# Optimization experiments

Measured on AMD Instinct MI355X. Metric: run time of the kernel, lower is better.

## Reference

```python
import jax, jax.numpy as jnp
import numpy as np

INPUT_LEN = 256
LATENT = 128
B, T = 64, 1024
# layer (in_dim, units): encoder: (256,256),(256,128); decoder: (128,256),(256,256)
LAYERS = [(INPUT_LEN, 2 * LATENT), (2 * LATENT, LATENT), (LATENT, 2 * LATENT), (2 * LATENT, INPUT_LEN)]


def _lstm_relu(xs, W, U, b):
    """Keras LSTM with activation='relu', recurrent_activation='sigmoid'.
    xs: [B,T,F]; W: [F,4H]; U: [H,4H]; b: [4H]; gate order i,f,g,o. Returns [B,T,H]."""
    Bsz = xs.shape[0]
    H = U.shape[0]
    h0 = jnp.zeros((Bsz, H), xs.dtype)
    c0 = jnp.zeros((Bsz, H), xs.dtype)
    # precompute input projection for all timesteps: [T,B,4H]
    zx = jnp.einsum('btf,fg->tbg', xs, W) + b

    def step(carry, zx_t):
        h, c = carry
        z = zx_t + h @ U
        i, f, g, o = jnp.split(z, 4, axis=-1)
        i = jax.nn.sigmoid(i)
        f = jax.nn.sigmoid(f)
        o = jax.nn.sigmoid(o)
        g = jax.nn.relu(g)
        c = f * c + i * g
        h = o * jax.nn.relu(c)
        return (h, c), h

    _, hs = jax.lax.scan(step, (h0, c0), zx)  # hs: [T,B,H]
    return jnp.swapaxes(hs, 0, 1)


def setup_inputs() -> dict:
    key = jax.random.key(0)
    ks = jax.random.split(key, 1 + 3 * len(LAYERS))
    d = {"x": jax.random.normal(ks[0], (B, T, INPUT_LEN), dtype=jnp.float32)}
    for li, (fin, h) in enumerate(LAYERS):
        kW, kU, kb = ks[1 + 3 * li], ks[2 + 3 * li], ks[3 + 3 * li]
        d[f"W{li+1}"] = jax.random.normal(kW, (fin, 4 * h), dtype=jnp.float32) * 0.05
        d[f"U{li+1}"] = jax.random.normal(kU, (h, 4 * h), dtype=jnp.float32) * 0.05
        d[f"b{li+1}"] = jnp.zeros((4 * h,), dtype=jnp.float32)
    return d


def reference(x, W1, U1, b1, W2, U2, b2, W3, U3, b3, W4, U4, b4):
    h = _lstm_relu(x, W1, U1, b1)   # encoder layer 1: [B,T,256]
    h = _lstm_relu(h, W2, U2, b2)   # encoder layer 2: [B,T,128]
    h = _lstm_relu(h, W3, U3, b3)   # decoder layer 1: [B,T,256]
    h = _lstm_relu(h, W4, U4, b4)   # decoder layer 2: [B,T,256]
    return h
```

## Files before the change

### kernel.cpp

```cpp
#include <hip/hip_runtime.h>
#include <hip/hip_bf16.h>


typedef __bf16 bf16x8 __attribute__((ext_vector_type(8)));
typedef float f32x4 __attribute__((ext_vector_type(4)));
typedef unsigned long long u64;

#define NWG 56
#define TSTEPS 1024
#define NSTEPS (TSTEPS + 3)

__device__ __forceinline__ f32x4 mfma16(bf16x8 a, bf16x8 b, f32x4 c) {
  return __builtin_amdgcn_mfma_f32_16x16x32_bf16(a, b, c, 0, 0, 0);
}

__device__ __forceinline__ float sigmoid_fast(float x) {
  return 1.0f / (1.0f + __expf(-x));
}

__device__ __forceinline__ bf16x8 load_frag_llc(const __bf16* p) {
  union { bf16x8 v; u64 d[2]; } u;
  u.d[0] = __hip_atomic_load((const u64*)p, __ATOMIC_RELAXED,
                             __HIP_MEMORY_SCOPE_AGENT);
  u.d[1] = __hip_atomic_load((const u64*)(p + 4), __ATOMIC_RELAXED,
                             __HIP_MEMORY_SCOPE_AGENT);
  return u.v;
}

__device__ __forceinline__ void store8_llc(__bf16* p, u64 v) {
  __hip_atomic_store((u64*)p, v, __ATOMIC_RELAXED, __HIP_MEMORY_SCOPE_AGENT);
}

__device__ __forceinline__ void poll_flags(unsigned* flags, unsigned s) {
  const int lane = threadIdx.x & 63;
  const int idx = (lane < NWG) ? lane : 0;
  while (true) {
    unsigned v = __hip_atomic_load(&flags[idx * 32], __ATOMIC_RELAXED,
                                   __HIP_MEMORY_SCOPE_AGENT);
    if (!__ballot(v < s)) break;
    __builtin_amdgcn_s_sleep(1);
  }
}

template <int F, int H, int LAYER>
__device__ void layer_loop(const float* __restrict__ xg,
                           const __bf16* __restrict__ xin,
                           const float* __restrict__ W,
                           const float* __restrict__ U,
                           const float* __restrict__ bias_g,
                           __bf16* __restrict__ hbuf,
                           float* __restrict__ out,
                           unsigned* flags, int wg, int slice, __bf16* smem) {
  constexpr int KW = F / 32;
  constexpr int KU = H / 32;
  constexpr int FOURH = 4 * H;
  const int tid = threadIdx.x;
  const int wave = tid >> 6;
  const int lane = tid & 63;
  const int l15 = lane & 15;
  const int q = lane >> 4;
  const int hcol = slice * 16 + l15;
  const int brow = wave * 16;

  float bz[4];
#pragma unroll
  for (int nt = 0; nt < 4; ++nt) bz[nt] = bias_g[nt * H + hcol];

  bf16x8 wf[4][KW];
  bf16x8 uf[4][KU];
  for (int idx = tid; idx < F * 64; idx += 256) {
    int k = idx >> 6, c = idx & 63;
    int col = (c >> 4) * H + slice * 16 + (c & 15);
    smem[c * F + k] = (__bf16)W[k * FOURH + col];
  }
  __syncthreads();
#pragma unroll
  for (int nt = 0; nt < 4; ++nt)
#pragma unroll
    for (int kk = 0; kk < KW; ++kk)
      wf[nt][kk] = *(const bf16x8*)&smem[(nt * 16 + l15) * F + kk * 32 + q * 8];
  __syncthreads();
  for (int idx = tid; idx < H * 64; idx += 256) {
    int k = idx >> 6, c = idx & 63;
    int col = (c >> 4) * H + slice * 16 + (c & 15);
    smem[c * H + k] = (__bf16)U[k * FOURH + col];
  }
  __syncthreads();
#pragma unroll
  for (int nt = 0; nt < 4; ++nt)
#pragma unroll
    for (int kk = 0; kk < KU; ++kk)
      uf[nt][kk] = *(const bf16x8*)&smem[(nt * 16 + l15) * H + kk * 32 + q * 8];
  __syncthreads();

  __bf16* hlds = smem;

  float c_state[4] = {0.f, 0.f, 0.f, 0.f};

  for (int s = 0; s < NSTEPS; ++s) {
    const int t = s - (LAYER - 1);
    const bool active = (t >= 0) & (t < TSTEPS);
    poll_flags(flags, (unsigned)s);
    float hv[4];
    if (active) {
      f32x4 acc[4] = {};
      if (LAYER == 1) {
        const float* xrow = xg + ((size_t)(brow + l15) * 1024 + t) * 256 + q * 8;
#pragma unroll
        for (int kk = 0; kk < KW; ++kk) {
          const float4* p = (const float4*)(xrow + kk * 32);
          float4 a0 = p[0], a1 = p[1];
          bf16x8 a;
          a[0] = (__bf16)a0.x; a[1] = (__bf16)a0.y;
          a[2] = (__bf16)a0.z; a[3] = (__bf16)a0.w;
          a[4] = (__bf16)a1.x; a[5] = (__bf16)a1.y;
          a[6] = (__bf16)a1.z; a[7] = (__bf16)a1.w;
#pragma unroll
          for (int nt = 0; nt < 4; ++nt) acc[nt] = mfma16(a, wf[nt][kk], acc[nt]);
        }
      } else {
        const __bf16* xr = xin + ((size_t)(t & 1) * 64 + brow + l15) * F + q * 8;
#pragma unroll
        for (int kk = 0; kk < KW; ++kk) {
          bf16x8 a = load_frag_llc(xr + kk * 32);
#pragma unroll
          for (int nt = 0; nt < 4; ++nt) acc[nt] = mfma16(a, wf[nt][kk], acc[nt]);
        }
      }
      if (t > 0) {
        const __bf16* hr = hbuf + ((size_t)((t - 1) & 1) * 64 + brow + l15) * H + q * 8;
#pragma unroll
        for (int kk = 0; kk < KU; ++kk) {
          bf16x8 a = load_frag_llc(hr + kk * 32);
#pragma unroll
          for (int nt = 0; nt < 4; ++nt) acc[nt] = mfma16(a, uf[nt][kk], acc[nt]);
        }
      }
#pragma unroll
      for (int r = 0; r < 4; ++r) {
        float zi = acc[0][r] + bz[0];
        float zf = acc[1][r] + bz[1];
        float zg = acc[2][r] + bz[2];
        float zo = acc[3][r] + bz[3];
        float ig = sigmoid_fast(zi);
        float fg = sigmoid_fast(zf);
        float gg = fmaxf(zg, 0.0f);
        float og = sigmoid_fast(zo);
        float cn = fg * c_state[r] + ig * gg;
        c_state[r] = cn;
        hv[r] = og * fmaxf(cn, 0.0f);
        hlds[(brow + q * 4 + r) * 16 + l15] = (__bf16)hv[r];
      }
    }
    __syncthreads();
    if (active) {
      int row = tid >> 2, cg = tid & 3;
      u64 v = *(const u64*)&hlds[row * 16 + cg * 4];
      store8_llc(hbuf + ((size_t)(t & 1) * 64 + row) * H + slice * 16 + cg * 4, v);
      if (LAYER == 4) {
#pragma unroll
        for (int r = 0; r < 4; ++r) {
          int b = brow + q * 4 + r;
          out[((size_t)b * 1024 + t) * 256 + hcol] = hv[r];
        }
      }
    }
    __syncthreads();
    if (tid == 0)
      __hip_atomic_store(&flags[wg * 32], (unsigned)(s + 1), __ATOMIC_RELAXED,
                         __HIP_MEMORY_SCOPE_AGENT);
  }
}

struct KParams {
  const float* x;
  const float* W1; const float* U1; const float* b1;
  const float* W2; const float* U2; const float* b2;
  const float* W3; const float* U3; const float* b3;
  const float* W4; const float* U4; const float* b4;
  float* out;
  unsigned* flags;
  void* h1; void* h2; void* h3; void* h4;
};

__global__ __launch_bounds__(256, 1) void lstm_kernel(KParams p) {
  __shared__ __align__(16) __bf16 smem[64 * 256];
  int wg = blockIdx.x;
  if (wg < 16)
    layer_loop<256, 256, 1>(p.x, nullptr, p.W1, p.U1, p.b1, (__bf16*)p.h1,
                            nullptr, p.flags, wg, wg, smem);
  else if (wg < 24)
    layer_loop<256, 128, 2>(nullptr, (const __bf16*)p.h1, p.W2, p.U2, p.b2,
                            (__bf16*)p.h2, nullptr, p.flags, wg, wg - 16, smem);
  else if (wg < 40)
    layer_loop<128, 256, 3>(nullptr, (const __bf16*)p.h2, p.W3, p.U3, p.b3,
                            (__bf16*)p.h3, nullptr, p.flags, wg, wg - 24, smem);
  else
    layer_loop<256, 256, 4>(nullptr, (const __bf16*)p.h3, p.W4, p.U4, p.b4,
                            (__bf16*)p.h4, p.out, p.flags, wg, wg - 40, smem);
}

extern "C" void kernel_launch(void* const* d_in, const int* in_sizes, int n_in,
                              void* d_out, int out_size, void* d_ws, size_t ws_size,
                              hipStream_t stream) {
  unsigned char* ws = (unsigned char*)d_ws;
  KParams p;
  p.x  = (const float*)d_in[0];
  p.W1 = (const float*)d_in[1];  p.U1 = (const float*)d_in[2];  p.b1 = (const float*)d_in[3];
  p.W2 = (const float*)d_in[4];  p.U2 = (const float*)d_in[5];  p.b2 = (const float*)d_in[6];
  p.W3 = (const float*)d_in[7];  p.U3 = (const float*)d_in[8];  p.b3 = (const float*)d_in[9];
  p.W4 = (const float*)d_in[10]; p.U4 = (const float*)d_in[11]; p.b4 = (const float*)d_in[12];
  p.out = (float*)d_out;
  p.flags = (unsigned*)ws;
  size_t off = 8192;
  p.h1 = (void*)(ws + off); off += (size_t)2 * 64 * 256 * 2;
  p.h2 = (void*)(ws + off); off += (size_t)2 * 64 * 128 * 2;
  p.h3 = (void*)(ws + off); off += (size_t)2 * 64 * 256 * 2;
  p.h4 = (void*)(ws + off);

  hipMemsetAsync(d_ws, 0, 8192, stream);

  lstm_kernel<<<dim3(NWG), dim3(256), 0, stream>>>(p);
}
```

Before: 8.022 ms.

## Narrow per-step barrier to neighbor layers, prefetch x, defer output stores

```diff
diff --git a/kernel.cpp b/kernel.cpp
--- a/kernel.cpp
+++ b/kernel.cpp
@@ -9,6 +9,9 @@
 #define NWG 56
 #define TSTEPS 1024
 #define NSTEPS (TSTEPS + 3)
+
+__device__ __constant__ const int kFlagCnt[6]  = {0, 16, 8, 16, 16, 0};
+__device__ __constant__ const int kFlagBase[6] = {0, 0, 32, 64, 96, 0};
 
 __device__ __forceinline__ f32x4 mfma16(bf16x8 a, bf16x8 b, f32x4 c) {
   return __builtin_amdgcn_mfma_f32_16x16x32_bf16(a, b, c, 0, 0, 0);
@@ -31,14 +34,25 @@
   __hip_atomic_store((u64*)p, v, __ATOMIC_RELAXED, __HIP_MEMORY_SCOPE_AGENT);
 }
 
-__device__ __forceinline__ void poll_flags(unsigned* flags, unsigned s) {
+template <int LAYER>
+__device__ __forceinline__ void wait_deps(unsigned* flags, unsigned s) {
+  constexpr int n1 = (LAYER >= 2) ? ((LAYER - 1 == 2) ? 8 : 16) : 0;
+  constexpr int n2 = (LAYER == 2) ? 8 : 16;
+  constexpr int n3 = (LAYER <= 3) ? ((LAYER + 1 == 2) ? 8 : 16) : 0;
+  constexpr int b1 = (LAYER >= 2) ? (LAYER - 2) * 32 : 0;
+  constexpr int b2 = (LAYER - 1) * 32;
+  constexpr int b3 = (LAYER <= 3) ? LAYER * 32 : 0;
   const int lane = threadIdx.x & 63;
-  const int idx = (lane < NWG) ? lane : 0;
+  int fidx;
+  if (lane < n1) fidx = b1 + lane;
+  else if (lane < n1 + n2) fidx = b2 + (lane - n1);
+  else if (lane < n1 + n2 + n3) fidx = b3 + (lane - n1 - n2);
+  else fidx = b2;
+  unsigned* p = &flags[fidx];
   while (true) {
-    unsigned v = __hip_atomic_load(&flags[idx * 32], __ATOMIC_RELAXED,
+    unsigned v = __hip_atomic_load(p, __ATOMIC_RELAXED,
                                    __HIP_MEMORY_SCOPE_AGENT);
     if (!__ballot(v < s)) break;
-    __builtin_amdgcn_s_sleep(1);
   }
 }
 
@@ -50,10 +64,11 @@
                            const float* __restrict__ bias_g,
                            __bf16* __restrict__ hbuf,
                            float* __restrict__ out,
-                           unsigned* flags, int wg, int slice, __bf16* smem) {
+                           unsigned* flags, int slice, __bf16* smem) {
   constexpr int KW = F / 32;
   constexpr int KU = H / 32;
   constexpr int FOURH = 4 * H;
+  constexpr int MYFLAG_BASE = (LAYER - 1) * 32;
   const int tid = threadIdx.x;
   const int wave = tid >> 6;
   const int lane = tid & 63;
@@ -100,24 +115,34 @@
   for (int s = 0; s < NSTEPS; ++s) {
     const int t = s - (LAYER - 1);
     const bool active = (t >= 0) & (t < TSTEPS);
-    poll_flags(flags, (unsigned)s);
+
+    bf16x8 a_pre[(LAYER == 1) ? KW : 1];
+    if (LAYER == 1 && active) {
+      const float* xrow = xg + ((size_t)(brow + l15) * 1024 + t) * 256 + q * 8;
+#pragma unroll
+      for (int kk = 0; kk < KW; ++kk) {
+        const float4* p4 = (const float4*)(xrow + kk * 32);
+        float4 a0 = p4[0], a1 = p4[1];
+        bf16x8 a;
+        a[0] = (__bf16)a0.x; a[1] = (__bf16)a0.y;
+        a[2] = (__bf16)a0.z; a[3] = (__bf16)a0.w;
+        a[4] = (__bf16)a1.x; a[5] = (__bf16)a1.y;
+        a[6] = (__bf16)a1.z; a[7] = (__bf16)a1.w;
+        a_pre[kk] = a;
+      }
+    }
+
+    wait_deps<LAYER>(flags, (unsigned)s);
+
     float hv[4];
     if (active) {
       f32x4 acc[4] = {};
       if (LAYER == 1) {
-        const float* xrow = xg + ((size_t)(brow + l15) * 1024 + t) * 256 + q * 8;
-#pragma unroll
-        for (int kk = 0; kk < KW; ++kk) {
-          const float4* p = (const float4*)(xrow + kk * 32);
-          float4 a0 = p[0], a1 = p[1];
-          bf16x8 a;
-          a[0] = (__bf16)a0.x; a[1] = (__bf16)a0.y;
-          a[2] = (__bf16)a0.z; a[3] = (__bf16)a0.w;
-          a[4] = (__bf16)a1.x; a[5] = (__bf16)a1.y;
-          a[6] = (__bf16)a1.z; a[7] = (__bf16)a1.w;
-#pragma unroll
-          for (int nt = 0; nt < 4; ++nt) acc[nt] = mfma16(a, wf[nt][kk], acc[nt]);
-        }
+#pragma unroll
+        for (int kk = 0; kk < KW; ++kk)
+#pragma unroll
+          for (int nt = 0; nt < 4; ++nt)
+            acc[nt] = mfma16(a_pre[kk], wf[nt][kk], acc[nt]);
       } else {
         const __bf16* xr = xin + ((size_t)(t & 1) * 64 + brow + l15) * F + q * 8;
 #pragma unroll
@@ -157,18 +182,18 @@
       int row = tid >> 2, cg = tid & 3;
       u64 v = *(const u64*)&hlds[row * 16 + cg * 4];
       store8_llc(hbuf + ((size_t)(t & 1) * 64 + row) * H + slice * 16 + cg * 4, v);
-      if (LAYER == 4) {
-#pragma unroll
-        for (int r = 0; r < 4; ++r) {
-          int b = brow + q * 4 + r;
-          out[((size_t)b * 1024 + t) * 256 + hcol] = hv[r];
-        }
-      }
     }
     __syncthreads();
     if (tid == 0)
-      __hip_atomic_store(&flags[wg * 32], (unsigned)(s + 1), __ATOMIC_RELAXED,
-                         __HIP_MEMORY_SCOPE_AGENT);
+      __hip_atomic_store(&flags[MYFLAG_BASE + slice], (unsigned)(s + 1),
+                         __ATOMIC_RELAXED, __HIP_MEMORY_SCOPE_AGENT);
+    if (LAYER == 4 && active) {
+#pragma unroll
+      for (int r = 0; r < 4; ++r) {
+        int b = brow + q * 4 + r;
+        out[((size_t)b * 1024 + t) * 256 + hcol] = hv[r];
+      }
+    }
   }
 }
 
@@ -188,16 +213,16 @@
   int wg = blockIdx.x;
   if (wg < 16)
     layer_loop<256, 256, 1>(p.x, nullptr, p.W1, p.U1, p.b1, (__bf16*)p.h1,
-                            nullptr, p.flags, wg, wg, smem);
+                            nullptr, p.flags, wg, smem);
   else if (wg < 24)
     layer_loop<256, 128, 2>(nullptr, (const __bf16*)p.h1, p.W2, p.U2, p.b2,
-                            (__bf16*)p.h2, nullptr, p.flags, wg, wg - 16, smem);
+                            (__bf16*)p.h2, nullptr, p.flags, wg - 16, smem);
   else if (wg < 40)
     layer_loop<128, 256, 3>(nullptr, (const __bf16*)p.h2, p.W3, p.U3, p.b3,
-                            (__bf16*)p.h3, nullptr, p.flags, wg, wg - 24, smem);
+                            (__bf16*)p.h3, nullptr, p.flags, wg - 24, smem);
   else
     layer_loop<256, 256, 4>(nullptr, (const __bf16*)p.h3, p.W4, p.U4, p.b4,
-                            (__bf16*)p.h4, p.out, p.flags, wg, wg - 40, smem);
+                            (__bf16*)p.h4, p.out, p.flags, wg - 40, smem);
 }
 
 extern "C" void kernel_launch(void* const* d_in, const int* in_sizes, int n_in,
```

Result: no change. 7.952 ms (-0.9%).

## Replace global flag barrier with sentinel-tagged ring buffers and decoupled layer wavefront

Applied to the files above, without the earlier changes.

```diff
diff --git a/kernel.cpp b/kernel.cpp
--- a/kernel.cpp
+++ b/kernel.cpp
@@ -8,49 +8,34 @@
 
 #define NWG 56
 #define TSTEPS 1024
-#define NSTEPS (TSTEPS + 3)
+#define RDEPTH 64
+#define SENT (~0ull)
 
 __device__ __forceinline__ f32x4 mfma16(bf16x8 a, bf16x8 b, f32x4 c) {
   return __builtin_amdgcn_mfma_f32_16x16x32_bf16(a, b, c, 0, 0, 0);
 }
-
 __device__ __forceinline__ float sigmoid_fast(float x) {
   return 1.0f / (1.0f + __expf(-x));
 }
-
-__device__ __forceinline__ bf16x8 load_frag_llc(const __bf16* p) {
-  union { bf16x8 v; u64 d[2]; } u;
-  u.d[0] = __hip_atomic_load((const u64*)p, __ATOMIC_RELAXED,
-                             __HIP_MEMORY_SCOPE_AGENT);
-  u.d[1] = __hip_atomic_load((const u64*)(p + 4), __ATOMIC_RELAXED,
-                             __HIP_MEMORY_SCOPE_AGENT);
-  return u.v;
-}
-
+__device__ __forceinline__ u64 load8_llc(const __bf16* p) {
+  return __hip_atomic_load((const u64*)p, __ATOMIC_RELAXED,
+                           __HIP_MEMORY_SCOPE_AGENT);
+}
 __device__ __forceinline__ void store8_llc(__bf16* p, u64 v) {
   __hip_atomic_store((u64*)p, v, __ATOMIC_RELAXED, __HIP_MEMORY_SCOPE_AGENT);
 }
-
-__device__ __forceinline__ void poll_flags(unsigned* flags, unsigned s) {
-  const int lane = threadIdx.x & 63;
-  const int idx = (lane < NWG) ? lane : 0;
-  while (true) {
-    unsigned v = __hip_atomic_load(&flags[idx * 32], __ATOMIC_RELAXED,
-                                   __HIP_MEMORY_SCOPE_AGENT);
-    if (!__ballot(v < s)) break;
-    __builtin_amdgcn_s_sleep(1);
-  }
-}
-
-template <int F, int H, int LAYER>
-__device__ void layer_loop(const float* __restrict__ xg,
-                           const __bf16* __restrict__ xin,
-                           const float* __restrict__ W,
-                           const float* __restrict__ U,
-                           const float* __restrict__ bias_g,
-                           __bf16* __restrict__ hbuf,
-                           float* __restrict__ out,
-                           unsigned* flags, int wg, int slice, __bf16* smem) {
+__device__ __forceinline__ bf16x8 frag_of(u64 lo, u64 hi) {
+  union { bf16x8 v; u64 d[2]; } u; u.d[0] = lo; u.d[1] = hi; return u.v;
+}
+
+template <int F, int H, int LAYER, int NDOWN>
+__device__ void layer_run(const float* __restrict__ xg,
+                          const __bf16* __restrict__ rin,
+                          const float* __restrict__ W, const float* __restrict__ U,
+                          const float* __restrict__ bias,
+                          __bf16* __restrict__ rout,
+                          float* __restrict__ out,
+                          unsigned* flags, int slice, __bf16* smem) {
   constexpr int KW = F / 32;
   constexpr int KU = H / 32;
   constexpr int FOURH = 4 * H;
@@ -61,10 +46,11 @@
   const int q = lane >> 4;
   const int hcol = slice * 16 + l15;
   const int brow = wave * 16;
+  const int srow = tid >> 2, scg = tid & 3;
 
   float bz[4];
 #pragma unroll
-  for (int nt = 0; nt < 4; ++nt) bz[nt] = bias_g[nt * H + hcol];
+  for (int nt = 0; nt < 4; ++nt) bz[nt] = bias[nt * H + hcol];
 
   bf16x8 wf[4][KW];
   bf16x8 uf[4][KU];
@@ -97,77 +83,128 @@
 
   float c_state[4] = {0.f, 0.f, 0.f, 0.f};
 
-  for (int s = 0; s < NSTEPS; ++s) {
-    const int t = s - (LAYER - 1);
-    const bool active = (t >= 0) & (t < TSTEPS);
-    poll_flags(flags, (unsigned)s);
+  for (int t = 0; t < TSTEPS; ++t) {
+    if (NDOWN > 0 && (t & 15) == 0 && t >= 48) {
+      if (wave == 0) {
+        const bool act = lane < NDOWN;
+        unsigned* fp = &flags[((LAYER - 1) * 16 + (act ? lane : 0)) * 32];
+        while (true) {
+          unsigned v = __hip_atomic_load(fp, __ATOMIC_RELAXED,
+                                         __HIP_MEMORY_SCOPE_AGENT);
+          if (!__ballot(act && (int)v < t - 32)) break;
+        }
+      }
+      __syncthreads();
+    }
+    store8_llc(rout + ((size_t)((t + 1) & (RDEPTH - 1))) * 64 * H + srow * H +
+                   slice * 16 + scg * 4, SENT);
+    __syncthreads();
+
+    float4 xf[(LAYER == 1) ? 2 * KW : 1];
+    if (LAYER == 1) {
+      const float* xrow = xg + ((size_t)(brow + l15) * 1024 + t) * 256 + q * 8;
+#pragma unroll
+      for (int kk = 0; kk < KW; ++kk) {
+        const float4* p4 = (const float4*)(xrow + kk * 32);
+        xf[2 * kk] = p4[0];
+        xf[2 * kk + 1] = p4[1];
+      }
+    }
+    u64 rh[2 * KU];
+    u64 rx[(LAYER > 1) ? 2 * KW : 2];
+    const bool needr = (t > 0);
+    const __bf16* rr = rout + ((size_t)((t - 1) & (RDEPTH - 1))) * 64 * H +
+                       (brow + l15) * H + q * 8;
+    const __bf16* xr = (LAYER > 1)
+        ? rin + ((size_t)(t & (RDEPTH - 1))) * 64 * F + (brow + l15) * F + q * 8
+        : nullptr;
+    if (needr || LAYER > 1) {
+      while (true) {
+        bool bad = false;
+        if (needr) {
+#pragma unroll
+          for (int kk = 0; kk < KU; ++kk) {
+            rh[2 * kk] = load8_llc(rr + kk * 32);
+            rh[2 * kk + 1] = load8_llc(rr + kk * 32 + 4);
+          }
+        }
+        if (LAYER > 1) {
+#pragma unroll
+          for (int kk = 0; kk < KW; ++kk) {
+            rx[2 * kk] = load8_llc(xr + kk * 32);
+            rx[2 * kk + 1] = load8_llc(xr + kk * 32 + 4);
+          }
+        }
+        if (needr) {
+#pragma unroll
+          for (int j = 0; j < 2 * KU; ++j) bad |= (rh[j] == SENT);
+        }
+        if (LAYER > 1) {
+#pragma unroll
+          for (int j = 0; j < 2 * KW; ++j) bad |= (rx[j] == SENT);
+        }
+        if (!__ballot(bad)) break;
+      }
+    }
+
+    f32x4 acc[4] = {};
+#pragma unroll
+    for (int kk = 0; kk < KW; ++kk) {
+      bf16x8 a;
+      if (LAYER == 1) {
+        float4 a0 = xf[2 * kk], a1 = xf[2 * kk + 1];
+        a[0] = (__bf16)a0.x; a[1] = (__bf16)a0.y;
+        a[2] = (__bf16)a0.z; a[3] = (__bf16)a0.w;
+        a[4] = (__bf16)a1.x; a[5] = (__bf16)a1.y;
+        a[6] = (__bf16)a1.z; a[7] = (__bf16)a1.w;
+      } else {
+        a = frag_of(rx[2 * kk], rx[2 * kk + 1]);
+      }
+#pragma unroll
+      for (int nt = 0; nt < 4; ++nt) acc[nt] = mfma16(a, wf[nt][kk], acc[nt]);
+    }
+    if (needr) {
+#pragma unroll
+      for (int kk = 0; kk < KU; ++kk) {
+        bf16x8 a = frag_of(rh[2 * kk], rh[2 * kk + 1]);
+#pragma unroll
+        for (int nt = 0; nt < 4; ++nt) acc[nt] = mfma16(a, uf[nt][kk], acc[nt]);
+      }
+    }
+
     float hv[4];
-    if (active) {
-      f32x4 acc[4] = {};
-      if (LAYER == 1) {
-        const float* xrow = xg + ((size_t)(brow + l15) * 1024 + t) * 256 + q * 8;
-#pragma unroll
-        for (int kk = 0; kk < KW; ++kk) {
-          const float4* p = (const float4*)(xrow + kk * 32);
-          float4 a0 = p[0], a1 = p[1];
-          bf16x8 a;
-          a[0] = (__bf16)a0.x; a[1] = (__bf16)a0.y;
-          a[2] = (__bf16)a0.z; a[3] = (__bf16)a0.w;
-          a[4] = (__bf16)a1.x; a[5] = (__bf16)a1.y;
-          a[6] = (__bf16)a1.z; a[7] = (__bf16)a1.w;
-#pragma unroll
-          for (int nt = 0; nt < 4; ++nt) acc[nt] = mfma16(a, wf[nt][kk], acc[nt]);
-        }
-      } else {
-        const __bf16* xr = xin + ((size_t)(t & 1) * 64 + brow + l15) * F + q * 8;
-#pragma unroll
-        for (int kk = 0; kk < KW; ++kk) {
-          bf16x8 a = load_frag_llc(xr + kk * 32);
-#pragma unroll
-          for (int nt = 0; nt < 4; ++nt) acc[nt] = mfma16(a, wf[nt][kk], acc[nt]);
-        }
-      }
-      if (t > 0) {
-        const __bf16* hr = hbuf + ((size_t)((t - 1) & 1) * 64 + brow + l15) * H + q * 8;
-#pragma unroll
-        for (int kk = 0; kk < KU; ++kk) {
-          bf16x8 a = load_frag_llc(hr + kk * 32);
-#pragma unroll
-          for (int nt = 0; nt < 4; ++nt) acc[nt] = mfma16(a, uf[nt][kk], acc[nt]);
-        }
-      }
+#pragma unroll
+    for (int r = 0; r < 4; ++r) {
+      float zi = acc[0][r] + bz[0];
+      float zf = acc[1][r] + bz[1];
+      float zg = acc[2][r] + bz[2];
+      float zo = acc[3][r] + bz[3];
+      float ig = sigmoid_fast(zi);
+      float fg = sigmoid_fast(zf);
+      float gg = fmaxf(zg, 0.0f);
+      float og = sigmoid_fast(zo);
+      float cn = fg * c_state[r] + ig * gg;
+      c_state[r] = cn;
+      hv[r] = og * fmaxf(cn, 0.0f);
+      hlds[(brow + q * 4 + r) * 16 + l15] = (__bf16)hv[r];
+    }
+    __syncthreads();
+
+    {
+      u64 v = *(const u64*)&hlds[srow * 16 + scg * 4];
+      store8_llc(rout + ((size_t)(t & (RDEPTH - 1))) * 64 * H + srow * H +
+                     slice * 16 + scg * 4, v);
+    }
+    if (LAYER == 4) {
 #pragma unroll
       for (int r = 0; r < 4; ++r) {
-        float zi = acc[0][r] + bz[0];
-        float zf = acc[1][r] + bz[1];
-        float zg = acc[2][r] + bz[2];
-        float zo = acc[3][r] + bz[3];
-        float ig = sigmoid_fast(zi);
-        float fg = sigmoid_fast(zf);
-        float gg = fmaxf(zg, 0.0f);
-        float og = sigmoid_fast(zo);
-        float cn = fg * c_state[r] + ig * gg;
-        c_state[r] = cn;
-        hv[r] = og * fmaxf(cn, 0.0f);
-        hlds[(brow + q * 4 + r) * 16 + l15] = (__bf16)hv[r];
-      }
-    }
-    __syncthreads();
-    if (active) {
-      int row = tid >> 2, cg = tid & 3;
-      u64 v = *(const u64*)&hlds[row * 16 + cg * 4];
-      store8_llc(hbuf + ((size_t)(t & 1) * 64 + row) * H + slice * 16 + cg * 4, v);
-      if (LAYER == 4) {
-#pragma unroll
-        for (int r = 0; r < 4; ++r) {
-          int b = brow + q * 4 + r;
-          out[((size_t)b * 1024 + t) * 256 + hcol] = hv[r];
-        }
-      }
-    }
-    __syncthreads();
-    if (tid == 0)
-      __hip_atomic_store(&flags[wg * 32], (unsigned)(s + 1), __ATOMIC_RELAXED,
+        int b = brow + q * 4 + r;
+        out[((size_t)b * 1024 + t) * 256 + hcol] = hv[r];
+      }
+    }
+    if (LAYER > 1 && (t & 15) == 15 && tid == 0)
+      __hip_atomic_store(&flags[((LAYER - 2) * 16 + slice) * 32],
+                         (unsigned)(t + 1), __ATOMIC_RELAXED,
                          __HIP_MEMORY_SCOPE_AGENT);
   }
 }
@@ -180,24 +217,24 @@
   const float* W4; const float* U4; const float* b4;
   float* out;
   unsigned* flags;
-  void* h1; void* h2; void* h3; void* h4;
+  __bf16* r1; __bf16* r2; __bf16* r3; __bf16* r4;
 };
 
 __global__ __launch_bounds__(256, 1) void lstm_kernel(KParams p) {
   __shared__ __align__(16) __bf16 smem[64 * 256];
   int wg = blockIdx.x;
   if (wg < 16)
-    layer_loop<256, 256, 1>(p.x, nullptr, p.W1, p.U1, p.b1, (__bf16*)p.h1,
-                            nullptr, p.flags, wg, wg, smem);
+    layer_run<256, 256, 1, 8>(p.x, nullptr, p.W1, p.U1, p.b1, p.r1, nullptr,
+                              p.flags, wg, smem);
   else if (wg < 24)
-    layer_loop<256, 128, 2>(nullptr, (const __bf16*)p.h1, p.W2, p.U2, p.b2,
-                            (__bf16*)p.h2, nullptr, p.flags, wg, wg - 16, smem);
+    layer_run<256, 128, 2, 16>(nullptr, p.r1, p.W2, p.U2, p.b2, p.r2, nullptr,
+                               p.flags, wg - 16, smem);
   else if (wg < 40)
-    layer_loop<128, 256, 3>(nullptr, (const __bf16*)p.h2, p.W3, p.U3, p.b3,
-                            (__bf16*)p.h3, nullptr, p.flags, wg, wg - 24, smem);
+    layer_run<128, 256, 3, 16>(nullptr, p.r2, p.W3, p.U3, p.b3, p.r3, nullptr,
+                               p.flags, wg - 24, smem);
   else
-    layer_loop<256, 256, 4>(nullptr, (const __bf16*)p.h3, p.W4, p.U4, p.b4,
-                            (__bf16*)p.h4, p.out, p.flags, wg, wg - 40, smem);
+    layer_run<256, 256, 4, 0>(nullptr, p.r3, p.W4, p.U4, p.b4, p.r4, p.out,
+                              p.flags, wg - 40, smem);
 }
 
 extern "C" void kernel_launch(void* const* d_in, const int* in_sizes, int n_in,
@@ -212,13 +249,16 @@
   p.W4 = (const float*)d_in[10]; p.U4 = (const float*)d_in[11]; p.b4 = (const float*)d_in[12];
   p.out = (float*)d_out;
   p.flags = (unsigned*)ws;
-  size_t off = 8192;
-  p.h1 = (void*)(ws + off); off += (size_t)2 * 64 * 256 * 2;
-  p.h2 = (void*)(ws + off); off += (size_t)2 * 64 * 128 * 2;
-  p.h3 = (void*)(ws + off); off += (size_t)2 * 64 * 256 * 2;
-  p.h4 = (void*)(ws + off);
-
-  hipMemsetAsync(d_ws, 0, 8192, stream);
+  size_t off = 16384;
+  const size_t rbytes256 = (size_t)RDEPTH * 64 * 256 * 2;
+  const size_t rbytes128 = (size_t)RDEPTH * 64 * 128 * 2;
+  p.r1 = (__bf16*)(ws + off); off += rbytes256;
+  p.r2 = (__bf16*)(ws + off); off += rbytes128;
+  p.r3 = (__bf16*)(ws + off); off += rbytes256;
+  p.r4 = (__bf16*)(ws + off); off += rbytes256;
+
+  hipMemsetAsync(ws, 0, 16384, stream);
+  hipMemsetAsync(ws + 16384, 0xFF, off - 16384, stream);
 
   lstm_kernel<<<dim3(NWG), dim3(256), 0, stream>>>(p);
 }
```

New measurement: 7.518 ms. 6.3% less time.
